# Optimization experiments

Measured on AMD Instinct MI355X. Metric: run time of the kernel, lower is better.

## Reference

```python
import math
import jax, jax.numpy as jnp
import numpy as np

B, C, HH, WW = 1, 256, 64, 64
NUM_HEADS = 8
GROUPS = 8
EPS = 1e-5


def setup_inputs() -> dict:
    key = jax.random.key(0)
    ks = jax.random.split(key, 5)
    x = jax.random.normal(ks[0], (B, C, HH, WW), dtype=jnp.float32)
    gn_gamma = jnp.ones((C,), dtype=jnp.float32)
    gn_beta = jnp.zeros((C,), dtype=jnp.float32)
    qkv_w = jax.random.normal(ks[1], (3 * C, C), dtype=jnp.float32) / math.sqrt(C)
    qkv_b = jax.random.normal(ks[2], (3 * C,), dtype=jnp.float32) * 0.02
    proj_w = jax.random.normal(ks[3], (C, C), dtype=jnp.float32) / math.sqrt(C)
    proj_b = jax.random.normal(ks[4], (C,), dtype=jnp.float32) * 0.02
    return {"x": x, "gn_gamma": gn_gamma, "gn_beta": gn_beta,
            "qkv_w": qkv_w, "qkv_b": qkv_b, "proj_w": proj_w, "proj_b": proj_b}


def reference(x, gn_gamma, gn_beta, qkv_w, qkv_b, proj_w, proj_b):
    b, c, h, w = x.shape
    t = h * w
    xf = x.reshape(b, c, t)
    # GroupNorm(8, C): normalize over (C/8 channels x T spatial) per group
    xg = xf.reshape(b, GROUPS, (c // GROUPS) * t)
    mean = xg.mean(axis=-1, keepdims=True)
    var = xg.var(axis=-1, keepdims=True)
    xn = ((xg - mean) * jax.lax.rsqrt(var + EPS)).reshape(b, c, t)
    xn = xn * gn_gamma[:, None] + gn_beta[:, None]
    # 1x1 Conv1d C -> 3C is a channel matmul
    qkv = jnp.einsum('oc,bct->bot', qkv_w, xn) + qkv_b[:, None]  # [b, 3C, t]
    nh = NUM_HEADS
    ch = c // nh
    q, k, v = jnp.split(qkv, 3, axis=1)  # each [b, C, t]
    q = q.reshape(b * nh, ch, t)
    k = k.reshape(b * nh, ch, t)
    v = v.reshape(b * nh, ch, t)
    scale = 1.0 / math.sqrt(math.sqrt(ch))
    weight = jnp.einsum('bct,bcs->bts', q * scale, k * scale)  # [b*nh, t, t]
    weight = jax.nn.softmax(weight.astype(jnp.float32), axis=-1).astype(qkv.dtype)
    a = jnp.einsum('bts,bcs->bct', weight, v).reshape(b, c, t)
    hout = jnp.einsum('oc,bct->bot', proj_w, a) + proj_b[:, None]
    return x + hout.reshape(b, c, h, w)
```

## Files before the change

### kernel.cpp

```cpp
#include <hip/hip_runtime.h>
#include <hip/hip_bf16.h>
#include <math.h>

#define C_DIM 256
#define T_DIM 4096
#define NHEADS 8
#define NGROUPS 8
#define NSPLIT 4
#define SRANGE (T_DIM / NSPLIT)
#define NT (SRANGE / 64)

typedef __attribute__((ext_vector_type(8))) short bf16x8;
typedef __attribute__((ext_vector_type(4))) float f32x4;

#if __has_builtin(__builtin_amdgcn_exp2f)
#define EXP2(x) __builtin_amdgcn_exp2f(x)
#else
#define EXP2(x) exp2f(x)
#endif

#define MFMA16(a, b, c) __builtin_amdgcn_mfma_f32_16x16x32_bf16(a, b, c, 0, 0, 0)

#define WS_PSUM 0
#define WS_PSQ  256
#define WS_MEAN 512
#define WS_RSTD 520
#define WS_QT_F   1024
#define WS_KT_F   (WS_QT_F + 524288)
#define WS_VB_F   (WS_KT_F + 524288)
#define WS_WQB_F  (WS_VB_F + 524288)
#define WS_WPB_F  (WS_WQB_F + 98304)
#define WS_OP_F   (WS_WPB_F + 32768)
#define WS_L_F    (WS_OP_F + NSPLIT * 256 * 4096 / 2)

#define QSCALE 0.2550348527f

__device__ __forceinline__ ushort f2bf(float f) {
  union { float f; unsigned u; } v; v.f = f;
  return (ushort)((v.u + 0x7fffu + ((v.u >> 16) & 1u)) >> 16);
}

__device__ __forceinline__ float bf2f(ushort u) {
  union { unsigned u; float f; } v; v.u = ((unsigned)u) << 16;
  return v.f;
}

__device__ __forceinline__ uint pk2(float a, float b) {
  __hip_bfloat162 h = __float22bfloat162_rn(make_float2(a, b));
  union { __hip_bfloat162 h; uint u; } c; c.h = h; return c.u;
}

__global__ __launch_bounds__(256) void gn_partial(const float* __restrict__ x,
                                                  float* __restrict__ ws) {
  const int g = blockIdx.y;
  const int bx = blockIdx.x;
  const size_t base = (size_t)g * 131072 + (size_t)bx * 4096;
  float s = 0.f, s2 = 0.f;
  for (int i = threadIdx.x; i < 4096; i += 256) {
    float v = x[base + i];
    s += v;
    s2 += v * v;
  }
#pragma unroll
  for (int mask = 1; mask <= 32; mask <<= 1) {
    s += __shfl_xor(s, mask, 64);
    s2 += __shfl_xor(s2, mask, 64);
  }
  __shared__ float red[8];
  const int wid = threadIdx.x >> 6;
  if ((threadIdx.x & 63) == 0) { red[wid] = s; red[4 + wid] = s2; }
  __syncthreads();
  if (threadIdx.x == 0) {
    ws[WS_PSUM + g * 32 + bx] = red[0] + red[1] + red[2] + red[3];
    ws[WS_PSQ + g * 32 + bx] = red[4] + red[5] + red[6] + red[7];
  }
}

__global__ __launch_bounds__(256) void w2bf_gn(const float* __restrict__ wq,
                                               const float* __restrict__ wp,
                                               float* __restrict__ ws,
                                               ushort* __restrict__ wqb,
                                               ushort* __restrict__ wpb) {
  const int i4 = (blockIdx.x * 256 + threadIdx.x) * 4;
  const int n1 = 768 * 256;
  if (i4 < n1) {
    float4 v = *(const float4*)(wq + i4);
    union { ushort us[4]; uint2 u; } pk;
    pk.us[0] = f2bf(v.x); pk.us[1] = f2bf(v.y); pk.us[2] = f2bf(v.z); pk.us[3] = f2bf(v.w);
    *(uint2*)(wqb + i4) = pk.u;
  } else {
    const int j = i4 - n1;
    float4 v = *(const float4*)(wp + j);
    union { ushort us[4]; uint2 u; } pk;
    pk.us[0] = f2bf(v.x); pk.us[1] = f2bf(v.y); pk.us[2] = f2bf(v.z); pk.us[3] = f2bf(v.w);
    *(uint2*)(wpb + j) = pk.u;
  }
  if (blockIdx.x == 0) {
    const int g = threadIdx.x >> 5, idx = threadIdx.x & 31;
    float s = ws[WS_PSUM + g * 32 + idx];
    float s2 = ws[WS_PSQ + g * 32 + idx];
#pragma unroll
    for (int mask = 1; mask <= 16; mask <<= 1) {
      s += __shfl_xor(s, mask, 32);
      s2 += __shfl_xor(s2, mask, 32);
    }
    if (idx == 0) {
      const float inv_n = 1.0f / 131072.0f;
      float mean = s * inv_n;
      float var = s2 * inv_n - mean * mean;
      ws[WS_MEAN + g] = mean;
      ws[WS_RSTD + g] = rsqrtf(var + 1e-5f);
    }
  }
}

__global__ __launch_bounds__(512) void qkv_mfma(const float* __restrict__ x,
                                                const float* __restrict__ gamma,
                                                const float* __restrict__ beta,
                                                const float* __restrict__ ws,
                                                const ushort* __restrict__ wqb,
                                                const float* __restrict__ bias,
                                                ushort* __restrict__ qt,
                                                ushort* __restrict__ kt,
                                                ushort* __restrict__ vb) {
  const int t0 = blockIdx.x * 16;
  __shared__ ushort A[16 * 256];
  __shared__ float fg[256], fb[256];
  const int tid = threadIdx.x;
  if (tid < 256) {
    const int c = tid, gg = c >> 5;
    float rstd = ws[WS_RSTD + gg], mean = ws[WS_MEAN + gg];
    float fgv = gamma[c] * rstd;
    fg[c] = fgv; fb[c] = beta[c] - mean * fgv;
  }
  __syncthreads();
#pragma unroll
  for (int p = 0; p < 2; ++p) {
    const int idx = p * 512 + tid;
    const int c = idx >> 2;
    const int tin = (idx & 3) * 4;
    float4 xv = *(const float4*)(x + (size_t)c * T_DIM + t0 + tin);
    const float fgc = fg[c], fbc = fb[c];
    float xn[4] = {fmaf(xv.x, fgc, fbc), fmaf(xv.y, fgc, fbc),
                   fmaf(xv.z, fgc, fbc), fmaf(xv.w, fgc, fbc)};
#pragma unroll
    for (int i = 0; i < 4; ++i) {
      const int t = tin + i;
      A[t * 256 + (c ^ ((t & 7) << 3))] = f2bf(xn[i]);
    }
  }
  __syncthreads();

  const int w = tid >> 6, lane = tid & 63, l15 = lane & 15, g = lane >> 4;
  const int ob = w * 96;
  f32x4 acc[6] = {};
  const ushort* wrow[6];
#pragma unroll
  for (int j = 0; j < 6; ++j)
    wrow[j] = wqb + (size_t)(ob + j * 16 + l15) * 256;

  bf16x8 bc[6], bn[6];
#pragma unroll
  for (int j = 0; j < 6; ++j) bc[j] = *(const bf16x8*)(wrow[j] + 8 * g);

#pragma unroll
  for (int kk = 0; kk < 8; ++kk) {
    const bf16x8 af = *(const bf16x8*)(&A[l15 * 256 + ((kk * 32 + 8 * g) ^ ((l15 & 7) << 3))]);
    if (kk < 7) {
#pragma unroll
      for (int j = 0; j < 6; ++j) bn[j] = *(const bf16x8*)(wrow[j] + (kk + 1) * 32 + 8 * g);
    }
#pragma unroll
    for (int j = 0; j < 6; ++j)
      acc[j] = MFMA16(af, bc[j], acc[j]);
#pragma unroll
    for (int j = 0; j < 6; ++j) bc[j] = bn[j];
  }

#pragma unroll
  for (int j = 0; j < 6; ++j) {
    const int o = ob + j * 16 + l15;
    const float bo = bias[o];
    const int tb = t0 + 4 * g;
    if (o < 256) {
      const int hh = o >> 5, d = o & 31;
#pragma unroll
      for (int r = 0; r < 4; ++r)
        qt[((size_t)hh * T_DIM + tb + r) * 32 + d] = f2bf((acc[j][r] + bo) * QSCALE);
    } else if (o < 512) {
      const int oo = o - 256;
      const int hh = oo >> 5, d = oo & 31;
#pragma unroll
      for (int r = 0; r < 4; ++r)
        kt[((size_t)hh * T_DIM + tb + r) * 32 + d] = f2bf(acc[j][r] + bo);
    } else {
      union { ushort us[4]; uint2 u; } pk;
#pragma unroll
      for (int r = 0; r < 4; ++r) pk.us[r] = f2bf(acc[j][r] + bo);
      *(uint2*)(vb + (size_t)(o - 512) * T_DIM + tb) = pk.u;
    }
  }
}

__global__ __launch_bounds__(512, 4) void attn_fwd(const ushort* __restrict__ qt,
                                                   const ushort* __restrict__ kt,
                                                   const ushort* __restrict__ vb,
                                                   ushort* __restrict__ Op,
                                                   float* __restrict__ Lb) {
  const int bid = blockIdx.x;
  const int h = bid & 7;
  const int inner = bid >> 3;
  const int qb = inner & 15;
  const int z = inner >> 4;
  const int tid = threadIdx.x;
  const int w = tid >> 6, lane = tid & 63, l15 = lane & 15, g = lane >> 4;

  __shared__ ushort Klds[2][64 * 40];
  __shared__ ushort Vlds[2][32 * 72];
  __shared__ ushort Plds[8][16 * 144];

  const int t_a = qb * 256 + w * 16 + l15;
  const int t_b = t_a + 128;
  const bf16x8 qfa = *(const bf16x8*)(qt + ((size_t)(h * T_DIM + t_a) * 32 + 8 * g));
  const bf16x8 qfb = *(const bf16x8*)(qt + ((size_t)(h * T_DIM + t_b) * 32 + 8 * g));

  f32x4 Oa0 = {}, Oa1 = {}, Ob0 = {}, Ob1 = {};
  float la = 0.f, lb = 0.f;

  const int sbeg = z * SRANGE;
  const ushort* kgp = kt + (size_t)h * T_DIM * 32 + (size_t)(sbeg + (tid >> 3)) * 32 + (tid & 7) * 4;
  const ushort* vgp = vb + (size_t)(h * 32 + (tid >> 4)) * T_DIM + sbeg + (tid & 15) * 4;
  ushort* kw0 = &Klds[0][(tid >> 3) * 40 + (tid & 7) * 4];
  ushort* vw0 = &Vlds[0][(tid >> 4) * 72 + (tid & 15) * 4];
  {
    *(uint2*)kw0 = *(const uint2*)kgp;
    *(uint2*)vw0 = *(const uint2*)vgp;
  }
  __syncthreads();

  ushort* prow_a = &Plds[w][l15 * 144];
  ushort* prow_b = prow_a + 72;
  int cur = 0;
  for (int t = 0; t < NT; ++t) {
    uint2 kn, vn;
    const bool more = (t + 1 < NT);
    if (more) {
      kn = *(const uint2*)(kgp + (size_t)(t + 1) * 2048);
      vn = *(const uint2*)(vgp + (t + 1) * 64);
    }

    const ushort* kbase = &Klds[cur][0];
    const ushort* vbase = &Vlds[cur][0];
    const f32x4 z4 = {};
    const bf16x8 kf0 = *(const bf16x8*)(kbase + (0 * 16 + l15) * 40 + 8 * g);
    const bf16x8 kf1 = *(const bf16x8*)(kbase + (1 * 16 + l15) * 40 + 8 * g);
    const bf16x8 kf2 = *(const bf16x8*)(kbase + (2 * 16 + l15) * 40 + 8 * g);
    const bf16x8 kf3 = *(const bf16x8*)(kbase + (3 * 16 + l15) * 40 + 8 * g);
    __builtin_amdgcn_s_setprio(1);
    f32x4 sa0 = MFMA16(kf0, qfa, z4);
    f32x4 sa1 = MFMA16(kf1, qfa, z4);
    f32x4 sa2 = MFMA16(kf2, qfa, z4);
    f32x4 sa3 = MFMA16(kf3, qfa, z4);
    f32x4 sb0 = MFMA16(kf0, qfb, z4);
    f32x4 sb1 = MFMA16(kf1, qfb, z4);
    f32x4 sb2 = MFMA16(kf2, qfb, z4);
    f32x4 sb3 = MFMA16(kf3, qfb, z4);
    __builtin_amdgcn_s_setprio(0);

    {
      float p0, p1, p2, p3; uint2 pv; float rsum;
      p0 = EXP2(sa0[0]); p1 = EXP2(sa0[1]); p2 = EXP2(sa0[2]); p3 = EXP2(sa0[3]);
      rsum = (p0 + p1) + (p2 + p3);
      pv.x = pk2(p0, p1); pv.y = pk2(p2, p3);
      *(uint2*)(prow_a + 0 * 16 + 4 * g) = pv;
      p0 = EXP2(sa1[0]); p1 = EXP2(sa1[1]); p2 = EXP2(sa1[2]); p3 = EXP2(sa1[3]);
      rsum += (p0 + p1) + (p2 + p3);
      pv.x = pk2(p0, p1); pv.y = pk2(p2, p3);
      *(uint2*)(prow_a + 1 * 16 + 4 * g) = pv;
      p0 = EXP2(sa2[0]); p1 = EXP2(sa2[1]); p2 = EXP2(sa2[2]); p3 = EXP2(sa2[3]);
      rsum += (p0 + p1) + (p2 + p3);
      pv.x = pk2(p0, p1); pv.y = pk2(p2, p3);
      *(uint2*)(prow_a + 2 * 16 + 4 * g) = pv;
      p0 = EXP2(sa3[0]); p1 = EXP2(sa3[1]); p2 = EXP2(sa3[2]); p3 = EXP2(sa3[3]);
      rsum += (p0 + p1) + (p2 + p3);
      pv.x = pk2(p0, p1); pv.y = pk2(p2, p3);
      *(uint2*)(prow_a + 3 * 16 + 4 * g) = pv;
      la += rsum;
    }

    const bf16x8 vf00 = *(const bf16x8*)(vbase + (l15) * 72 + 8 * g);
    const bf16x8 vf01 = *(const bf16x8*)(vbase + (l15) * 72 + 32 + 8 * g);
    const bf16x8 vf10 = *(const bf16x8*)(vbase + (16 + l15) * 72 + 8 * g);
    const bf16x8 vf11 = *(const bf16x8*)(vbase + (16 + l15) * 72 + 32 + 8 * g);

    const bf16x8 pfa0 = *(const bf16x8*)(prow_a + 8 * g);
    const bf16x8 pfa1 = *(const bf16x8*)(prow_a + 32 + 8 * g);
    __builtin_amdgcn_s_setprio(1);
    Oa0 = MFMA16(vf00, pfa0, Oa0);
    Oa0 = MFMA16(vf01, pfa1, Oa0);
    Oa1 = MFMA16(vf10, pfa0, Oa1);
    Oa1 = MFMA16(vf11, pfa1, Oa1);
    __builtin_amdgcn_s_setprio(0);

    {
      float p0, p1, p2, p3; uint2 pv; float rsum;
      p0 = EXP2(sb0[0]); p1 = EXP2(sb0[1]); p2 = EXP2(sb0[2]); p3 = EXP2(sb0[3]);
      rsum = (p0 + p1) + (p2 + p3);
      pv.x = pk2(p0, p1); pv.y = pk2(p2, p3);
      *(uint2*)(prow_b + 0 * 16 + 4 * g) = pv;
      p0 = EXP2(sb1[0]); p1 = EXP2(sb1[1]); p2 = EXP2(sb1[2]); p3 = EXP2(sb1[3]);
      rsum += (p0 + p1) + (p2 + p3);
      pv.x = pk2(p0, p1); pv.y = pk2(p2, p3);
      *(uint2*)(prow_b + 1 * 16 + 4 * g) = pv;
      p0 = EXP2(sb2[0]); p1 = EXP2(sb2[1]); p2 = EXP2(sb2[2]); p3 = EXP2(sb2[3]);
      rsum += (p0 + p1) + (p2 + p3);
      pv.x = pk2(p0, p1); pv.y = pk2(p2, p3);
      *(uint2*)(prow_b + 2 * 16 + 4 * g) = pv;
      p0 = EXP2(sb3[0]); p1 = EXP2(sb3[1]); p2 = EXP2(sb3[2]); p3 = EXP2(sb3[3]);
      rsum += (p0 + p1) + (p2 + p3);
      pv.x = pk2(p0, p1); pv.y = pk2(p2, p3);
      *(uint2*)(prow_b + 3 * 16 + 4 * g) = pv;
      lb += rsum;
    }

    const bf16x8 pfb0 = *(const bf16x8*)(prow_b + 8 * g);
    const bf16x8 pfb1 = *(const bf16x8*)(prow_b + 32 + 8 * g);
    __builtin_amdgcn_s_setprio(1);
    Ob0 = MFMA16(vf00, pfb0, Ob0);
    Ob0 = MFMA16(vf01, pfb1, Ob0);
    Ob1 = MFMA16(vf10, pfb0, Ob1);
    Ob1 = MFMA16(vf11, pfb1, Ob1);
    __builtin_amdgcn_s_setprio(0);

    if (more) {
      *(uint2*)(kw0 + (cur ^ 1) * (64 * 40)) = kn;
      *(uint2*)(vw0 + (cur ^ 1) * (32 * 72)) = vn;
    }
    __syncthreads();
    cur ^= 1;
  }

  ushort* opz = Op + (size_t)(z * NHEADS + h) * 32 * T_DIM;
#pragma unroll
  for (int r = 0; r < 4; ++r) {
    const int d0 = 4 * g + r;
    opz[(size_t)d0 * T_DIM + t_a]        = f2bf(Oa0[r]);
    opz[(size_t)(16 + d0) * T_DIM + t_a] = f2bf(Oa1[r]);
    opz[(size_t)d0 * T_DIM + t_b]        = f2bf(Ob0[r]);
    opz[(size_t)(16 + d0) * T_DIM + t_b] = f2bf(Ob1[r]);
  }
  la += __shfl_xor(la, 16, 64);
  la += __shfl_xor(la, 32, 64);
  lb += __shfl_xor(lb, 16, 64);
  lb += __shfl_xor(lb, 32, 64);
  if (g == 0) {
    Lb[(size_t)(z * NHEADS + h) * T_DIM + t_a] = la;
    Lb[(size_t)(z * NHEADS + h) * T_DIM + t_b] = lb;
  }
}

__global__ __launch_bounds__(256) void proj_mfma(const ushort* __restrict__ Op,
                                                 const float* __restrict__ Lb,
                                                 const ushort* __restrict__ wpb,
                                                 const float* __restrict__ bias,
                                                 const float* __restrict__ x,
                                                 float* __restrict__ out) {
  const int t0 = blockIdx.x * 16;
  __shared__ ushort A[16 * 256];
  __shared__ float rinv[128];
  const int tid = threadIdx.x;
  if (tid < 128) {
    const int h = tid >> 4, tt = tid & 15;
    float l = 0.f;
#pragma unroll
    for (int zz = 0; zz < NSPLIT; ++zz)
      l += Lb[(size_t)(zz * NHEADS + h) * T_DIM + t0 + tt];
    rinv[tid] = 1.0f / l;
  }
  __syncthreads();
#pragma unroll
  for (int pass = 0; pass < 4; ++pass) {
    const int c = pass * 64 + (tid >> 2);
    const int h = c >> 5;
    const int tin = (tid & 3) * 4;
    float a4[4] = {0.f, 0.f, 0.f, 0.f};
#pragma unroll
    for (int zz = 0; zz < NSPLIT; ++zz) {
      uint2 v = *(const uint2*)(Op + (size_t)(zz * 256 + c) * T_DIM + t0 + tin);
      const ushort* us = (const ushort*)&v;
#pragma unroll
      for (int i = 0; i < 4; ++i) a4[i] += bf2f(us[i]);
    }
#pragma unroll
    for (int i = 0; i < 4; ++i) {
      const int t = tin + i;
      A[t * 256 + (c ^ ((t & 7) << 3))] = f2bf(a4[i] * rinv[(h << 4) | t]);
    }
  }
  __syncthreads();

  const int w = tid >> 6, lane = tid & 63, l15 = lane & 15, g = lane >> 4;
  const int o0 = blockIdx.y * 128 + w * 32;
  f32x4 acc[2] = {};
  const ushort* wrow[2];
#pragma unroll
  for (int j = 0; j < 2; ++j)
    wrow[j] = wpb + (size_t)(o0 + 16 * j + l15) * 256;

#pragma unroll
  for (int kk = 0; kk < 8; ++kk) {
    const bf16x8 af = *(const bf16x8*)(&A[l15 * 256 + ((kk * 32 + 8 * g) ^ ((l15 & 7) << 3))]);
#pragma unroll
    for (int j = 0; j < 2; ++j) {
      const bf16x8 bfr = *(const bf16x8*)(wrow[j] + kk * 32 + 8 * g);
      acc[j] = MFMA16(af, bfr, acc[j]);
    }
  }

#pragma unroll
  for (int j = 0; j < 2; ++j) {
    const int o = o0 + 16 * j + l15;
    const float bo = bias[o];
    const size_t base = (size_t)o * T_DIM + t0 + 4 * g;
    const float4 xr = *(const float4*)(x + base);
    float4 ov;
    ov.x = acc[j][0] + bo + xr.x;
    ov.y = acc[j][1] + bo + xr.y;
    ov.z = acc[j][2] + bo + xr.z;
    ov.w = acc[j][3] + bo + xr.w;
    *(float4*)(out + base) = ov;
  }
}

extern "C" void kernel_launch(void* const* d_in, const int* in_sizes, int n_in,
                              void* d_out, int out_size, void* d_ws, size_t ws_size,
                              hipStream_t stream) {
  const float* x      = (const float*)d_in[0];
  const float* gamma  = (const float*)d_in[1];
  const float* beta   = (const float*)d_in[2];
  const float* qkv_w  = (const float*)d_in[3];
  const float* qkv_b  = (const float*)d_in[4];
  const float* proj_w = (const float*)d_in[5];
  const float* proj_b = (const float*)d_in[6];
  float* out = (float*)d_out;
  float* ws  = (float*)d_ws;

  ushort* qt  = (ushort*)(ws + WS_QT_F);
  ushort* kt  = (ushort*)(ws + WS_KT_F);
  ushort* vb  = (ushort*)(ws + WS_VB_F);
  ushort* wqb = (ushort*)(ws + WS_WQB_F);
  ushort* wpb = (ushort*)(ws + WS_WPB_F);
  ushort* Op  = (ushort*)(ws + WS_OP_F);
  float*  Lb  = ws + WS_L_F;

  gn_partial<<<dim3(32, NGROUPS), 256, 0, stream>>>(x, ws);
  w2bf_gn<<<256, 256, 0, stream>>>(qkv_w, proj_w, ws, wqb, wpb);
  qkv_mfma<<<256, 512, 0, stream>>>(x, gamma, beta, ws, wqb, qkv_b, qt, kt, vb);
  attn_fwd<<<NHEADS * 16 * NSPLIT, 512, 0, stream>>>(qt, kt, vb, Op, Lb);
  proj_mfma<<<dim3(256, 2), 256, 0, stream>>>(Op, Lb, wpb, proj_b, x, out);
}
```

Baseline: 73.63 us.

## Keep softmax probabilities in registers and fuse GroupNorm stats into prep

The attention kernel no longer round-trips the exponentiated scores through shared memory. Instead it permutes the K rows written to LDS so the QK^T MFMA output layout lines up directly with the B-operand layout of the PV MFMA, and packs the probabilities straight into bf16 registers. Separately, the GroupNorm partial-sum kernel is merged into the weight-conversion kernel, and the final mean/rstd reduction moves into each qkv block, which removes one launch. The cost is a redundant stats reduction in every qkv block, and correctness depends on the row permutation matching the MFMA layouts exactly.

```diff
diff --git a/kernel.cpp b/kernel.cpp
--- a/kernel.cpp
+++ b/kernel.cpp
@@ -23,8 +23,6 @@
 
 #define WS_PSUM 0
 #define WS_PSQ  256
-#define WS_MEAN 512
-#define WS_RSTD 520
 #define WS_QT_F   1024
 #define WS_KT_F   (WS_QT_F + 524288)
 #define WS_VB_F   (WS_KT_F + 524288)
@@ -50,37 +48,12 @@
   union { __hip_bfloat162 h; uint u; } c; c.h = h; return c.u;
 }
 
-__global__ __launch_bounds__(256) void gn_partial(const float* __restrict__ x,
-                                                  float* __restrict__ ws) {
-  const int g = blockIdx.y;
-  const int bx = blockIdx.x;
-  const size_t base = (size_t)g * 131072 + (size_t)bx * 4096;
-  float s = 0.f, s2 = 0.f;
-  for (int i = threadIdx.x; i < 4096; i += 256) {
-    float v = x[base + i];
-    s += v;
-    s2 += v * v;
-  }
-#pragma unroll
-  for (int mask = 1; mask <= 32; mask <<= 1) {
-    s += __shfl_xor(s, mask, 64);
-    s2 += __shfl_xor(s2, mask, 64);
-  }
-  __shared__ float red[8];
-  const int wid = threadIdx.x >> 6;
-  if ((threadIdx.x & 63) == 0) { red[wid] = s; red[4 + wid] = s2; }
-  __syncthreads();
-  if (threadIdx.x == 0) {
-    ws[WS_PSUM + g * 32 + bx] = red[0] + red[1] + red[2] + red[3];
-    ws[WS_PSQ + g * 32 + bx] = red[4] + red[5] + red[6] + red[7];
-  }
-}
-
-__global__ __launch_bounds__(256) void w2bf_gn(const float* __restrict__ wq,
-                                               const float* __restrict__ wp,
-                                               float* __restrict__ ws,
-                                               ushort* __restrict__ wqb,
-                                               ushort* __restrict__ wpb) {
+__global__ __launch_bounds__(256) void prep(const float* __restrict__ x,
+                                            const float* __restrict__ wq,
+                                            const float* __restrict__ wp,
+                                            float* __restrict__ ws,
+                                            ushort* __restrict__ wqb,
+                                            ushort* __restrict__ wpb) {
   const int i4 = (blockIdx.x * 256 + threadIdx.x) * 4;
   const int n1 = 768 * 256;
   if (i4 < n1) {
@@ -95,22 +68,27 @@
     pk.us[0] = f2bf(v.x); pk.us[1] = f2bf(v.y); pk.us[2] = f2bf(v.z); pk.us[3] = f2bf(v.w);
     *(uint2*)(wpb + j) = pk.u;
   }
-  if (blockIdx.x == 0) {
-    const int g = threadIdx.x >> 5, idx = threadIdx.x & 31;
-    float s = ws[WS_PSUM + g * 32 + idx];
-    float s2 = ws[WS_PSQ + g * 32 + idx];
-#pragma unroll
-    for (int mask = 1; mask <= 16; mask <<= 1) {
-      s += __shfl_xor(s, mask, 32);
-      s2 += __shfl_xor(s2, mask, 32);
-    }
-    if (idx == 0) {
-      const float inv_n = 1.0f / 131072.0f;
-      float mean = s * inv_n;
-      float var = s2 * inv_n - mean * mean;
-      ws[WS_MEAN + g] = mean;
-      ws[WS_RSTD + g] = rsqrtf(var + 1e-5f);
-    }
+  const int g = blockIdx.x >> 5;
+  const int bx = blockIdx.x & 31;
+  const size_t base = (size_t)g * 131072 + (size_t)bx * 4096;
+  float s = 0.f, s2 = 0.f;
+  for (int i = threadIdx.x; i < 4096; i += 256) {
+    float v = x[base + i];
+    s += v;
+    s2 += v * v;
+  }
+#pragma unroll
+  for (int mask = 1; mask <= 32; mask <<= 1) {
+    s += __shfl_xor(s, mask, 64);
+    s2 += __shfl_xor(s2, mask, 64);
+  }
+  __shared__ float red[8];
+  const int wid = threadIdx.x >> 6;
+  if ((threadIdx.x & 63) == 0) { red[wid] = s; red[4 + wid] = s2; }
+  __syncthreads();
+  if (threadIdx.x == 0) {
+    ws[WS_PSUM + g * 32 + bx] = red[0] + red[1] + red[2] + red[3];
+    ws[WS_PSQ + g * 32 + bx] = red[4] + red[5] + red[6] + red[7];
   }
 }
 
@@ -126,12 +104,30 @@
   const int t0 = blockIdx.x * 16;
   __shared__ ushort A[16 * 256];
   __shared__ float fg[256], fb[256];
+  __shared__ float sm_stat[16];
   const int tid = threadIdx.x;
   if (tid < 256) {
+    const int gg = tid >> 5, i = tid & 31;
+    float s = ws[WS_PSUM + gg * 32 + i];
+    float s2 = ws[WS_PSQ + gg * 32 + i];
+#pragma unroll
+    for (int mask = 1; mask <= 16; mask <<= 1) {
+      s += __shfl_xor(s, mask, 32);
+      s2 += __shfl_xor(s2, mask, 32);
+    }
+    if (i == 0) {
+      const float inv_n = 1.0f / 131072.0f;
+      float mean = s * inv_n;
+      float var = s2 * inv_n - mean * mean;
+      sm_stat[gg] = mean;
+      sm_stat[8 + gg] = rsqrtf(var + 1e-5f);
+    }
+  }
+  __syncthreads();
+  if (tid < 256) {
     const int c = tid, gg = c >> 5;
-    float rstd = ws[WS_RSTD + gg], mean = ws[WS_MEAN + gg];
-    float fgv = gamma[c] * rstd;
-    fg[c] = fgv; fb[c] = beta[c] - mean * fgv;
+    float fgv = gamma[c] * sm_stat[8 + gg];
+    fg[c] = fgv; fb[c] = beta[c] - sm_stat[gg] * fgv;
   }
   __syncthreads();
 #pragma unroll
@@ -217,7 +213,6 @@
 
   __shared__ ushort Klds[2][64 * 40];
   __shared__ ushort Vlds[2][32 * 72];
-  __shared__ ushort Plds[8][16 * 144];
 
   const int t_a = qb * 256 + w * 16 + l15;
   const int t_b = t_a + 128;
@@ -228,9 +223,12 @@
   float la = 0.f, lb = 0.f;
 
   const int sbeg = z * SRANGE;
-  const ushort* kgp = kt + (size_t)h * T_DIM * 32 + (size_t)(sbeg + (tid >> 3)) * 32 + (tid & 7) * 4;
+  const int p_row = tid >> 3;
+  const int q5 = p_row & 31;
+  const int sm_row = (p_row & 32) + 16 * ((q5 >> 2) & 1) + 4 * (q5 >> 3) + (q5 & 3);
+  const ushort* kgp = kt + (size_t)h * T_DIM * 32 + (size_t)(sbeg + p_row) * 32 + (tid & 7) * 4;
   const ushort* vgp = vb + (size_t)(h * 32 + (tid >> 4)) * T_DIM + sbeg + (tid & 15) * 4;
-  ushort* kw0 = &Klds[0][(tid >> 3) * 40 + (tid & 7) * 4];
+  ushort* kw0 = &Klds[0][sm_row * 40 + (tid & 7) * 4];
   ushort* vw0 = &Vlds[0][(tid >> 4) * 72 + (tid & 15) * 4];
   {
     *(uint2*)kw0 = *(const uint2*)kgp;
@@ -238,8 +236,6 @@
   }
   __syncthreads();
 
-  ushort* prow_a = &Plds[w][l15 * 144];
-  ushort* prow_b = prow_a + 72;
   int cur = 0;
   for (int t = 0; t < NT; ++t) {
     uint2 kn, vn;
@@ -267,69 +263,52 @@
     f32x4 sb3 = MFMA16(kf3, qfb, z4);
     __builtin_amdgcn_s_setprio(0);
 
-    {
-      float p0, p1, p2, p3; uint2 pv; float rsum;
-      p0 = EXP2(sa0[0]); p1 = EXP2(sa0[1]); p2 = EXP2(sa0[2]); p3 = EXP2(sa0[3]);
-      rsum = (p0 + p1) + (p2 + p3);
-      pv.x = pk2(p0, p1); pv.y = pk2(p2, p3);
-      *(uint2*)(prow_a + 0 * 16 + 4 * g) = pv;
-      p0 = EXP2(sa1[0]); p1 = EXP2(sa1[1]); p2 = EXP2(sa1[2]); p3 = EXP2(sa1[3]);
-      rsum += (p0 + p1) + (p2 + p3);
-      pv.x = pk2(p0, p1); pv.y = pk2(p2, p3);
-      *(uint2*)(prow_a + 1 * 16 + 4 * g) = pv;
-      p0 = EXP2(sa2[0]); p1 = EXP2(sa2[1]); p2 = EXP2(sa2[2]); p3 = EXP2(sa2[3]);
-      rsum += (p0 + p1) + (p2 + p3);
-      pv.x = pk2(p0, p1); pv.y = pk2(p2, p3);
-      *(uint2*)(prow_a + 2 * 16 + 4 * g) = pv;
-      p0 = EXP2(sa3[0]); p1 = EXP2(sa3[1]); p2 = EXP2(sa3[2]); p3 = EXP2(sa3[3]);
-      rsum += (p0 + p1) + (p2 + p3);
-      pv.x = pk2(p0, p1); pv.y = pk2(p2, p3);
-      *(uint2*)(prow_a + 3 * 16 + 4 * g) = pv;
-      la += rsum;
-    }
-
     const bf16x8 vf00 = *(const bf16x8*)(vbase + (l15) * 72 + 8 * g);
     const bf16x8 vf01 = *(const bf16x8*)(vbase + (l15) * 72 + 32 + 8 * g);
     const bf16x8 vf10 = *(const bf16x8*)(vbase + (16 + l15) * 72 + 8 * g);
     const bf16x8 vf11 = *(const bf16x8*)(vbase + (16 + l15) * 72 + 32 + 8 * g);
 
-    const bf16x8 pfa0 = *(const bf16x8*)(prow_a + 8 * g);
-    const bf16x8 pfa1 = *(const bf16x8*)(prow_a + 32 + 8 * g);
+    union { uint u[4]; bf16x8 v; } fa0, fa1, fb0, fb1;
+    {
+      float p0, p1, p2, p3, p4, p5, p6, p7;
+      p0 = EXP2(sa0[0]); p1 = EXP2(sa0[1]); p2 = EXP2(sa0[2]); p3 = EXP2(sa0[3]);
+      p4 = EXP2(sa1[0]); p5 = EXP2(sa1[1]); p6 = EXP2(sa1[2]); p7 = EXP2(sa1[3]);
+      la += ((p0 + p1) + (p2 + p3)) + ((p4 + p5) + (p6 + p7));
+      fa0.u[0] = pk2(p0, p1); fa0.u[1] = pk2(p2, p3);
+      fa0.u[2] = pk2(p4, p5); fa0.u[3] = pk2(p6, p7);
+      p0 = EXP2(sa2[0]); p1 = EXP2(sa2[1]); p2 = EXP2(sa2[2]); p3 = EXP2(sa2[3]);
+      p4 = EXP2(sa3[0]); p5 = EXP2(sa3[1]); p6 = EXP2(sa3[2]); p7 = EXP2(sa3[3]);
+      la += ((p0 + p1) + (p2 + p3)) + ((p4 + p5) + (p6 + p7));
+      fa1.u[0] = pk2(p0, p1); fa1.u[1] = pk2(p2, p3);
+      fa1.u[2] = pk2(p4, p5); fa1.u[3] = pk2(p6, p7);
+    }
+
     __builtin_amdgcn_s_setprio(1);
-    Oa0 = MFMA16(vf00, pfa0, Oa0);
-    Oa0 = MFMA16(vf01, pfa1, Oa0);
-    Oa1 = MFMA16(vf10, pfa0, Oa1);
-    Oa1 = MFMA16(vf11, pfa1, Oa1);
+    Oa0 = MFMA16(vf00, fa0.v, Oa0);
+    Oa0 = MFMA16(vf01, fa1.v, Oa0);
+    Oa1 = MFMA16(vf10, fa0.v, Oa1);
+    Oa1 = MFMA16(vf11, fa1.v, Oa1);
     __builtin_amdgcn_s_setprio(0);
 
     {
-      float p0, p1, p2, p3; uint2 pv; float rsum;
+      float p0, p1, p2, p3, p4, p5, p6, p7;
       p0 = EXP2(sb0[0]); p1 = EXP2(sb0[1]); p2 = EXP2(sb0[2]); p3 = EXP2(sb0[3]);
-      rsum = (p0 + p1) + (p2 + p3);
-      pv.x = pk2(p0, p1); pv.y = pk2(p2, p3);
-      *(uint2*)(prow_b + 0 * 16 + 4 * g) = pv;
-      p0 = EXP2(sb1[0]); p1 = EXP2(sb1[1]); p2 = EXP2(sb1[2]); p3 = EXP2(sb1[3]);
-      rsum += (p0 + p1) + (p2 + p3);
-      pv.x = pk2(p0, p1); pv.y = pk2(p2, p3);
-      *(uint2*)(prow_b + 1 * 16 + 4 * g) = pv;
+      p4 = EXP2(sb1[0]); p5 = EXP2(sb1[1]); p6 = EXP2(sb1[2]); p7 = EXP2(sb1[3]);
+      lb += ((p0 + p1) + (p2 + p3)) + ((p4 + p5) + (p6 + p7));
+      fb0.u[0] = pk2(p0, p1); fb0.u[1] = pk2(p2, p3);
+      fb0.u[2] = pk2(p4, p5); fb0.u[3] = pk2(p6, p7);
       p0 = EXP2(sb2[0]); p1 = EXP2(sb2[1]); p2 = EXP2(sb2[2]); p3 = EXP2(sb2[3]);
-      rsum += (p0 + p1) + (p2 + p3);
-      pv.x = pk2(p0, p1); pv.y = pk2(p2, p3);
-      *(uint2*)(prow_b + 2 * 16 + 4 * g) = pv;
-      p0 = EXP2(sb3[0]); p1 = EXP2(sb3[1]); p2 = EXP2(sb3[2]); p3 = EXP2(sb3[3]);
-      rsum += (p0 + p1) + (p2 + p3);
-      pv.x = pk2(p0, p1); pv.y = pk2(p2, p3);
-      *(uint2*)(prow_b + 3 * 16 + 4 * g) = pv;
-      lb += rsum;
-    }
-
-    const bf16x8 pfb0 = *(const bf16x8*)(prow_b + 8 * g);
-    const bf16x8 pfb1 = *(const bf16x8*)(prow_b + 32 + 8 * g);
+      p4 = EXP2(sb3[0]); p5 = EXP2(sb3[1]); p6 = EXP2(sb3[2]); p7 = EXP2(sb3[3]);
+      lb += ((p0 + p1) + (p2 + p3)) + ((p4 + p5) + (p6 + p7));
+      fb1.u[0] = pk2(p0, p1); fb1.u[1] = pk2(p2, p3);
+      fb1.u[2] = pk2(p4, p5); fb1.u[3] = pk2(p6, p7);
+    }
+
     __builtin_amdgcn_s_setprio(1);
-    Ob0 = MFMA16(vf00, pfb0, Ob0);
-    Ob0 = MFMA16(vf01, pfb1, Ob0);
-    Ob1 = MFMA16(vf10, pfb0, Ob1);
-    Ob1 = MFMA16(vf11, pfb1, Ob1);
+    Ob0 = MFMA16(vf00, fb0.v, Ob0);
+    Ob0 = MFMA16(vf01, fb1.v, Ob0);
+    Ob1 = MFMA16(vf10, fb0.v, Ob1);
+    Ob1 = MFMA16(vf11, fb1.v, Ob1);
     __builtin_amdgcn_s_setprio(0);
 
     if (more) {
@@ -453,8 +432,7 @@
   ushort* Op  = (ushort*)(ws + WS_OP_F);
   float*  Lb  = ws + WS_L_F;
 
-  gn_partial<<<dim3(32, NGROUPS), 256, 0, stream>>>(x, ws);
-  w2bf_gn<<<256, 256, 0, stream>>>(qkv_w, proj_w, ws, wqb, wpb);
+  prep<<<256, 256, 0, stream>>>(x, qkv_w, proj_w, ws, wqb, wpb);
   qkv_mfma<<<256, 512, 0, stream>>>(x, gamma, beta, ws, wqb, qkv_b, qt, kt, vb);
   attn_fwd<<<NHEADS * 16 * NSPLIT, 512, 0, stream>>>(qt, kt, vb, Op, Lb);
   proj_mfma<<<dim3(256, 2), 256, 0, stream>>>(Op, Lb, wpb, proj_b, x, out);
```

Result: faster. 67.42 us (-8.4%).
